# Performance work log

Measured on AMD Instinct MI355X. Metric: run time of the kernel, lower is better.

Reference implementation:

```python
import jax, jax.numpy as jnp
import numpy as np

ALPHA = 0.9
BETA = 0.85
THRESHOLD = 1.0
SIM_TIME = 128  # simulation_time
SURR_SCALE = 100.0


@jax.custom_vjp
def spike(x):
    # Heaviside step (SurrGradSpike.forward)
    return (x > 0).astype(x.dtype)

def _spike_fwd(x):
    return spike(x), x

def _spike_bwd(x, g):
    # fast-sigmoid surrogate gradient (Zenke & Ganguli 2018)
    return (g / (SURR_SCALE * jnp.abs(x) + 1.0) ** 2,)

spike.defvjp(_spike_fwd, _spike_bwd)


def setup_inputs() -> dict:
    key = jax.random.key(0)
    k0, k1, k2, k3 = jax.random.split(key, 4)
    B, IN, H = 16384, 128, 512
    inputs = jax.random.normal(k0, (B, IN), dtype=jnp.float32)
    # architecture[0] is doubled by the pos/neg input split -> W0: [2*IN, H]
    W0 = jax.random.normal(k1, (2 * IN, H), dtype=jnp.float32)
    W1 = jax.random.normal(k2, (H, H), dtype=jnp.float32)
    W2 = jax.random.normal(k3, (H, H), dtype=jnp.float32)
    return {"inputs": inputs, "W0": W0, "W1": W1, "W2": W2}


def _forward(inputs, Ws):
    # split input into positive / rectified-negative halves, concat on feature dim
    x = jnp.concatenate([jnp.maximum(inputs, 0.0), jnp.maximum(-inputs, 0.0)], axis=1)
    B = x.shape[0]
    L = len(Ws)
    syn0 = tuple(jnp.zeros((B, W.shape[1]), x.dtype) for W in Ws)
    mem0 = tuple(jnp.zeros((B, W.shape[1]), x.dtype) for W in Ws)

    def step(carry, _):
        syn, mem = carry
        new_syn, new_mem = [], []
        prev_spk = None
        for l, W in enumerate(Ws):
            h = jnp.einsum("bi,ij->bj", x if l == 0 else prev_spk, W)
            s = h if l == 0 else ALPHA * syn[l] + h  # layer 0: 0*syn + h
            m = BETA * mem[l] + s
            if l < L - 1:
                mthr = m - THRESHOLD
                prev_spk = spike(mthr)
                m = jnp.where(mthr > 0, 0.0, m)  # reset spiked membranes
            new_syn.append(s)
            new_mem.append(m)
        return (tuple(new_syn), tuple(new_mem)), None

    # t=0 in the original only records zeros and skips the update -> run T-1 steps
    (syn, mem), _ = jax.lax.scan(step, (syn0, mem0), None, length=SIM_TIME - 1)
    # returned value = mem_rec[-1][-1]: last layer membrane at final timestep
    return mem[-1]


def reference(inputs, W0, W1, W2):
    return _forward(inputs, (W0, W1, W2))
```

## Files before the change

kernel.cpp:

```cpp
#include <hip/hip_runtime.h>
#include <stdint.h>


typedef __attribute__((ext_vector_type(2))) float f32x2;
typedef __attribute__((ext_vector_type(4))) float f32x4;

#define ALPHA 0.9f
#define BETA 0.85f
#define NSTEPS 127
#define WGT 1024
#define ROWS 32
#define CPAD 36
#define HPAD 516

#define LIF_L0(M, H, SP) { float _m = BETA * (M) + (H); \
    const bool _b = (_m - 1.0f) > 0.0f; (M) = _b ? 0.0f : _m; \
    (SP) = _b ? 1.0f : 0.0f; }
#define LIF_MID(S, M, A, SP) { (S) = ALPHA * (S) + (A); \
    float _m = BETA * (M) + (S); const bool _b = (_m - 1.0f) > 0.0f; \
    (M) = _b ? 0.0f : _m; (SP) = _b ? 1.0f : 0.0f; }
#define LIF_OUT(S, M, A) { (S) = ALPHA * (S) + (A); (M) = BETA * (M) + (S); }

__global__ __launch_bounds__(WGT, 4)
void dsnn_kernel(const float* __restrict__ x,
                 const float* __restrict__ W0,
                 const float* __restrict__ W1,
                 const float* __restrict__ W2,
                 float* __restrict__ out)
{
    __shared__ float spkbuf[512 * CPAD];
    __shared__ float h0buf[ROWS * HPAD];

    const int t  = threadIdx.x;
    const int c2 = (t & 255) * 2;
    const int g  = (t >> 8) * 8;
    const int r0 = blockIdx.x * ROWS;

    for (int k = t; k < 256 * ROWS; k += WGT) {
        const int i = k >> 5;
        const int r = k & 31;
        const float v = (i < 128) ? x[(size_t)(r0 + r) * 128 + i]
                                  : -x[(size_t)(r0 + r) * 128 + (i - 128)];
        spkbuf[i * CPAD + r] = fmaxf(v, 0.0f);
    }
    __syncthreads();

    float acc[8][2];

    auto gemm = [&](const float* Wcol, int K) {
        #pragma unroll 2
        for (int j = 0; j < K; ++j) {
            const float* sb = spkbuf + j * CPAD + g;
            const f32x4 sA = *(const f32x4*)(sb);
            const f32x4 sB = *(const f32x4*)(sb + 4);
            const f32x2 wv = *(const f32x2*)(Wcol + (size_t)j * 512);
            #pragma unroll
            for (int rr = 0; rr < 4; ++rr) {
                acc[rr][0]     = fmaf(sA[rr], wv.x, acc[rr][0]);
                acc[rr][1]     = fmaf(sA[rr], wv.y, acc[rr][1]);
                acc[4 + rr][0] = fmaf(sB[rr], wv.x, acc[4 + rr][0]);
                acc[4 + rr][1] = fmaf(sB[rr], wv.y, acc[4 + rr][1]);
            }
        }
    };

    #pragma unroll
    for (int r = 0; r < 8; ++r) { acc[r][0] = 0.0f; acc[r][1] = 0.0f; }
    gemm(W0 + c2, 256);
    #pragma unroll
    for (int r = 0; r < 8; ++r) {
        f32x2 hv = { acc[r][0], acc[r][1] };
        *(f32x2*)(h0buf + (g + r) * HPAD + c2) = hv;
    }
    __syncthreads();

    float m0[8][2], s1[8][2], m1[8][2], s2[8][2], m2[8][2];
    #pragma unroll
    for (int r = 0; r < 8; ++r)
        #pragma unroll
        for (int cc = 0; cc < 2; ++cc) {
            m0[r][cc] = 0.f; s1[r][cc] = 0.f; m1[r][cc] = 0.f;
            s2[r][cc] = 0.f; m2[r][cc] = 0.f;
        }

    for (int step = 0; step < NSTEPS; ++step) {
        {
            f32x4 svA[2], svB[2];
            #pragma unroll
            for (int rr = 0; rr < 4; ++rr) {
                const f32x2 hva = *(const f32x2*)(h0buf + (g + rr) * HPAD + c2);
                const f32x2 hvb = *(const f32x2*)(h0buf + (g + 4 + rr) * HPAD + c2);
                LIF_L0(m0[rr][0], hva.x, svA[0][rr]);
                LIF_L0(m0[rr][1], hva.y, svA[1][rr]);
                LIF_L0(m0[4 + rr][0], hvb.x, svB[0][rr]);
                LIF_L0(m0[4 + rr][1], hvb.y, svB[1][rr]);
            }
            #pragma unroll
            for (int cc = 0; cc < 2; ++cc) {
                *(f32x4*)(spkbuf + (c2 + cc) * CPAD + g)     = svA[cc];
                *(f32x4*)(spkbuf + (c2 + cc) * CPAD + g + 4) = svB[cc];
            }
        }
        __syncthreads();

        #pragma unroll
        for (int r = 0; r < 8; ++r) { acc[r][0] = 0.0f; acc[r][1] = 0.0f; }
        gemm(W1 + c2, 512);
        __syncthreads();

        {
            f32x4 svA[2], svB[2];
            #pragma unroll
            for (int rr = 0; rr < 4; ++rr) {
                LIF_MID(s1[rr][0], m1[rr][0], acc[rr][0], svA[0][rr]);
                LIF_MID(s1[rr][1], m1[rr][1], acc[rr][1], svA[1][rr]);
                LIF_MID(s1[4 + rr][0], m1[4 + rr][0], acc[4 + rr][0], svB[0][rr]);
                LIF_MID(s1[4 + rr][1], m1[4 + rr][1], acc[4 + rr][1], svB[1][rr]);
            }
            #pragma unroll
            for (int cc = 0; cc < 2; ++cc) {
                *(f32x4*)(spkbuf + (c2 + cc) * CPAD + g)     = svA[cc];
                *(f32x4*)(spkbuf + (c2 + cc) * CPAD + g + 4) = svB[cc];
            }
        }
        __syncthreads();

        #pragma unroll
        for (int r = 0; r < 8; ++r) { acc[r][0] = 0.0f; acc[r][1] = 0.0f; }
        gemm(W2 + c2, 512);
        #pragma unroll
        for (int r = 0; r < 8; ++r) {
            LIF_OUT(s2[r][0], m2[r][0], acc[r][0]);
            LIF_OUT(s2[r][1], m2[r][1], acc[r][1]);
        }
        __syncthreads();
    }

    #pragma unroll
    for (int r = 0; r < 8; ++r) {
        f32x2 ov = { m2[r][0], m2[r][1] };
        *(f32x2*)(out + (size_t)(r0 + g + r) * 512 + c2) = ov;
    }
}

extern "C" void kernel_launch(void* const* d_in, const int* in_sizes, int n_in,
                              void* d_out, int out_size, void* d_ws, size_t ws_size,
                              hipStream_t stream) {
    const float* inputs = (const float*)d_in[0];
    const float* W0     = (const float*)d_in[1];
    const float* W1     = (const float*)d_in[2];
    const float* W2     = (const float*)d_in[3];
    float* out          = (float*)d_out;

    dim3 grid(16384 / ROWS);
    dim3 block(WGT);
    dsnn_kernel<<<grid, block, 0, stream>>>(inputs, W0, W1, W2, out);
}
```

Baseline: 32.99 ms.

## Double-buffer spike LDS, keep layer-0 current in registers, prefetch weights

Splits the shared spike buffer into two buffers, one for layer-1 spikes and one for layer-2 spikes. This lets two of the four barriers per timestep be removed, because successive writers and readers no longer touch the same buffer. The constant layer-0 input current is now held in registers instead of being re-read from LDS every step. The GEMM loop also software-prefetches the next weight pair and is unrolled more deeply. The cost is higher register pressure from 16 extra live floats, which may hurt occupancy under launch_bounds(1024,4).

```diff
diff --git a/kernel.cpp b/kernel.cpp
--- a/kernel.cpp
+++ b/kernel.cpp
@@ -11,7 +11,6 @@
 #define WGT 1024
 #define ROWS 32
 #define CPAD 36
-#define HPAD 516
 
 #define LIF_L0(M, H, SP) { float _m = BETA * (M) + (H); \
     const bool _b = (_m - 1.0f) > 0.0f; (M) = _b ? 0.0f : _m; \
@@ -28,8 +27,8 @@
                  const float* __restrict__ W2,
                  float* __restrict__ out)
 {
-    __shared__ float spkbuf[512 * CPAD];
-    __shared__ float h0buf[ROWS * HPAD];
+    __shared__ float bufP[512 * CPAD];
+    __shared__ float bufQ[512 * CPAD];
 
     const int t  = threadIdx.x;
     const int c2 = (t & 255) * 2;
@@ -41,37 +40,49 @@
         const int r = k & 31;
         const float v = (i < 128) ? x[(size_t)(r0 + r) * 128 + i]
                                   : -x[(size_t)(r0 + r) * 128 + (i - 128)];
-        spkbuf[i * CPAD + r] = fmaxf(v, 0.0f);
+        bufP[i * CPAD + r] = fmaxf(v, 0.0f);
     }
     __syncthreads();
 
     float acc[8][2];
 
-    auto gemm = [&](const float* Wcol, int K) {
-        #pragma unroll 2
-        for (int j = 0; j < K; ++j) {
-            const float* sb = spkbuf + j * CPAD + g;
+    auto gemm = [&](const float* Wcol, const float* sbuf, int K) {
+        const float* sb = sbuf + g;
+        f32x2 pw = *(const f32x2*)(Wcol);
+        #pragma unroll 4
+        for (int j = 0; j < K - 1; ++j) {
+            const f32x2 cw = pw;
+            pw = *(const f32x2*)(Wcol + (size_t)(j + 1) * 512);
             const f32x4 sA = *(const f32x4*)(sb);
             const f32x4 sB = *(const f32x4*)(sb + 4);
-            const f32x2 wv = *(const f32x2*)(Wcol + (size_t)j * 512);
+            sb += CPAD;
             #pragma unroll
             for (int rr = 0; rr < 4; ++rr) {
-                acc[rr][0]     = fmaf(sA[rr], wv.x, acc[rr][0]);
-                acc[rr][1]     = fmaf(sA[rr], wv.y, acc[rr][1]);
-                acc[4 + rr][0] = fmaf(sB[rr], wv.x, acc[4 + rr][0]);
-                acc[4 + rr][1] = fmaf(sB[rr], wv.y, acc[4 + rr][1]);
+                acc[rr][0]     = fmaf(sA[rr], cw.x, acc[rr][0]);
+                acc[rr][1]     = fmaf(sA[rr], cw.y, acc[rr][1]);
+                acc[4 + rr][0] = fmaf(sB[rr], cw.x, acc[4 + rr][0]);
+                acc[4 + rr][1] = fmaf(sB[rr], cw.y, acc[4 + rr][1]);
+            }
+        }
+        {
+            const f32x4 sA = *(const f32x4*)(sb);
+            const f32x4 sB = *(const f32x4*)(sb + 4);
+            #pragma unroll
+            for (int rr = 0; rr < 4; ++rr) {
+                acc[rr][0]     = fmaf(sA[rr], pw.x, acc[rr][0]);
+                acc[rr][1]     = fmaf(sA[rr], pw.y, acc[rr][1]);
+                acc[4 + rr][0] = fmaf(sB[rr], pw.x, acc[4 + rr][0]);
+                acc[4 + rr][1] = fmaf(sB[rr], pw.y, acc[4 + rr][1]);
             }
         }
     };
 
     #pragma unroll
     for (int r = 0; r < 8; ++r) { acc[r][0] = 0.0f; acc[r][1] = 0.0f; }
-    gemm(W0 + c2, 256);
+    gemm(W0 + c2, bufP, 256);
+    float h0r[8][2];
     #pragma unroll
-    for (int r = 0; r < 8; ++r) {
-        f32x2 hv = { acc[r][0], acc[r][1] };
-        *(f32x2*)(h0buf + (g + r) * HPAD + c2) = hv;
-    }
+    for (int r = 0; r < 8; ++r) { h0r[r][0] = acc[r][0]; h0r[r][1] = acc[r][1]; }
     __syncthreads();
 
     float m0[8][2], s1[8][2], m1[8][2], s2[8][2], m2[8][2];
@@ -88,25 +99,22 @@
             f32x4 svA[2], svB[2];
             #pragma unroll
             for (int rr = 0; rr < 4; ++rr) {
-                const f32x2 hva = *(const f32x2*)(h0buf + (g + rr) * HPAD + c2);
-                const f32x2 hvb = *(const f32x2*)(h0buf + (g + 4 + rr) * HPAD + c2);
-                LIF_L0(m0[rr][0], hva.x, svA[0][rr]);
-                LIF_L0(m0[rr][1], hva.y, svA[1][rr]);
-                LIF_L0(m0[4 + rr][0], hvb.x, svB[0][rr]);
-                LIF_L0(m0[4 + rr][1], hvb.y, svB[1][rr]);
+                LIF_L0(m0[rr][0], h0r[rr][0], svA[0][rr]);
+                LIF_L0(m0[rr][1], h0r[rr][1], svA[1][rr]);
+                LIF_L0(m0[4 + rr][0], h0r[4 + rr][0], svB[0][rr]);
+                LIF_L0(m0[4 + rr][1], h0r[4 + rr][1], svB[1][rr]);
             }
             #pragma unroll
             for (int cc = 0; cc < 2; ++cc) {
-                *(f32x4*)(spkbuf + (c2 + cc) * CPAD + g)     = svA[cc];
-                *(f32x4*)(spkbuf + (c2 + cc) * CPAD + g + 4) = svB[cc];
+                *(f32x4*)(bufP + (c2 + cc) * CPAD + g)     = svA[cc];
+                *(f32x4*)(bufP + (c2 + cc) * CPAD + g + 4) = svB[cc];
             }
         }
         __syncthreads();
 
         #pragma unroll
         for (int r = 0; r < 8; ++r) { acc[r][0] = 0.0f; acc[r][1] = 0.0f; }
-        gemm(W1 + c2, 512);
-        __syncthreads();
+        gemm(W1 + c2, bufP, 512);
 
         {
             f32x4 svA[2], svB[2];
@@ -119,21 +127,20 @@
             }
             #pragma unroll
             for (int cc = 0; cc < 2; ++cc) {
-                *(f32x4*)(spkbuf + (c2 + cc) * CPAD + g)     = svA[cc];
-                *(f32x4*)(spkbuf + (c2 + cc) * CPAD + g + 4) = svB[cc];
+                *(f32x4*)(bufQ + (c2 + cc) * CPAD + g)     = svA[cc];
+                *(f32x4*)(bufQ + (c2 + cc) * CPAD + g + 4) = svB[cc];
             }
         }
         __syncthreads();
 
         #pragma unroll
         for (int r = 0; r < 8; ++r) { acc[r][0] = 0.0f; acc[r][1] = 0.0f; }
-        gemm(W2 + c2, 512);
+        gemm(W2 + c2, bufQ, 512);
         #pragma unroll
         for (int r = 0; r < 8; ++r) {
             LIF_OUT(s2[r][0], m2[r][0], acc[r][0]);
             LIF_OUT(s2[r][1], m2[r][1], acc[r][1]);
         }
-        __syncthreads();
     }
 
     #pragma unroll
```

Measured after the change: 40.06 ms. +21.4%, slower.

## Stage weight tiles into LDS with async global_load_lds double buffering

Applied to the files above, without the earlier changes.

Weight rows are no longer read by every thread straight from global memory. Each 16-row weight tile is now copied into a double-buffered LDS array with global_load_lds, and the copy of the next tile overlaps compute on the current one. To free LDS for this, the layer-0 input current is kept in the output buffer in global memory instead of in shared memory. The change adds a barrier per tile and global reads of the h0 values on every step, and it relies on each thread reading back its own h0 writes.

```diff
diff --git a/kernel.cpp b/kernel.cpp
--- a/kernel.cpp
+++ b/kernel.cpp
@@ -11,7 +11,10 @@
 #define WGT 1024
 #define ROWS 32
 #define CPAD 36
-#define HPAD 516
+#define BK 16
+
+#define GAS __attribute__((address_space(1)))
+#define LAS __attribute__((address_space(3)))
 
 #define LIF_L0(M, H, SP) { float _m = BETA * (M) + (H); \
     const bool _b = (_m - 1.0f) > 0.0f; (M) = _b ? 0.0f : _m; \
@@ -29,12 +32,14 @@
                  float* __restrict__ out)
 {
     __shared__ float spkbuf[512 * CPAD];
-    __shared__ float h0buf[ROWS * HPAD];
+    __shared__ float Wb[2][BK * 512];
 
-    const int t  = threadIdx.x;
-    const int c2 = (t & 255) * 2;
-    const int g  = (t >> 8) * 8;
-    const int r0 = blockIdx.x * ROWS;
+    const int t    = threadIdx.x;
+    const int lane = t & 63;
+    const int w    = t >> 6;
+    const int c2   = (t & 255) * 2;
+    const int g    = (t >> 8) * 8;
+    const int r0   = blockIdx.x * ROWS;
 
     for (int k = t; k < 256 * ROWS; k += WGT) {
         const int i = k >> 5;
@@ -43,17 +48,22 @@
                                   : -x[(size_t)(r0 + r) * 128 + (i - 128)];
         spkbuf[i * CPAD + r] = fmaxf(v, 0.0f);
     }
-    __syncthreads();
+
+    auto stage = [&](const float* Wsrc, int jbase, int buf) {
+        const float* gp = Wsrc + (size_t)(jbase + w) * 512 + lane * 4;
+        float* lp = &Wb[buf][w * 512 + lane * 4];
+        __builtin_amdgcn_global_load_lds((const GAS void*)gp,        (LAS void*)lp,        16, 0, 0);
+        __builtin_amdgcn_global_load_lds((const GAS void*)(gp+256),  (LAS void*)(lp+256),  16, 0, 0);
+    };
 
     float acc[8][2];
 
-    auto gemm = [&](const float* Wcol, int K) {
-        #pragma unroll 2
-        for (int j = 0; j < K; ++j) {
-            const float* sb = spkbuf + j * CPAD + g;
-            const f32x4 sA = *(const f32x4*)(sb);
-            const f32x4 sB = *(const f32x4*)(sb + 4);
-            const f32x2 wv = *(const f32x2*)(Wcol + (size_t)j * 512);
+    auto compute16 = [&](const float* wb, const float* sb) {
+        #pragma unroll
+        for (int jl = 0; jl < BK; ++jl) {
+            const f32x4 sA = *(const f32x4*)(sb + jl * CPAD);
+            const f32x4 sB = *(const f32x4*)(sb + jl * CPAD + 4);
+            const f32x2 wv = *(const f32x2*)(wb + jl * 512);
             #pragma unroll
             for (int rr = 0; rr < 4; ++rr) {
                 acc[rr][0]     = fmaf(sA[rr], wv.x, acc[rr][0]);
@@ -64,15 +74,25 @@
         }
     };
 
+    auto gemm = [&](const float* Wsrc, int K) {
+        const int NB = K / BK;
+        stage(Wsrc, 0, 0);
+        __syncthreads();
+        for (int b = 0; b < NB; ++b) {
+            if (b + 1 < NB) stage(Wsrc, (b + 1) * BK, (b + 1) & 1);
+            compute16(&Wb[b & 1][c2], spkbuf + b * (BK * CPAD) + g);
+            __syncthreads();
+        }
+    };
+
     #pragma unroll
     for (int r = 0; r < 8; ++r) { acc[r][0] = 0.0f; acc[r][1] = 0.0f; }
-    gemm(W0 + c2, 256);
+    gemm(W0, 256);
     #pragma unroll
     for (int r = 0; r < 8; ++r) {
         f32x2 hv = { acc[r][0], acc[r][1] };
-        *(f32x2*)(h0buf + (g + r) * HPAD + c2) = hv;
+        *(f32x2*)(out + (size_t)(r0 + g + r) * 512 + c2) = hv;
     }
-    __syncthreads();
 
     float m0[8][2], s1[8][2], m1[8][2], s2[8][2], m2[8][2];
     #pragma unroll
@@ -88,8 +108,8 @@
             f32x4 svA[2], svB[2];
             #pragma unroll
             for (int rr = 0; rr < 4; ++rr) {
-                const f32x2 hva = *(const f32x2*)(h0buf + (g + rr) * HPAD + c2);
-                const f32x2 hvb = *(const f32x2*)(h0buf + (g + 4 + rr) * HPAD + c2);
+                const f32x2 hva = *(const f32x2*)(out + (size_t)(r0 + g + rr) * 512 + c2);
+                const f32x2 hvb = *(const f32x2*)(out + (size_t)(r0 + g + 4 + rr) * 512 + c2);
                 LIF_L0(m0[rr][0], hva.x, svA[0][rr]);
                 LIF_L0(m0[rr][1], hva.y, svA[1][rr]);
                 LIF_L0(m0[4 + rr][0], hvb.x, svB[0][rr]);
@@ -105,8 +125,7 @@
 
         #pragma unroll
         for (int r = 0; r < 8; ++r) { acc[r][0] = 0.0f; acc[r][1] = 0.0f; }
-        gemm(W1 + c2, 512);
-        __syncthreads();
+        gemm(W1, 512);
 
         {
             f32x4 svA[2], svB[2];
@@ -127,13 +146,12 @@
 
         #pragma unroll
         for (int r = 0; r < 8; ++r) { acc[r][0] = 0.0f; acc[r][1] = 0.0f; }
-        gemm(W2 + c2, 512);
+        gemm(W2, 512);
         #pragma unroll
         for (int r = 0; r < 8; ++r) {
             LIF_OUT(s2[r][0], m2[r][0], acc[r][0]);
             LIF_OUT(s2[r][1], m2[r][1], acc[r][1]);
         }
-        __syncthreads();
     }
 
     #pragma unroll
```

Result: slower. 36.33 ms (+10.1%).
